# Kernel tuning notes

Measured on AMD Instinct MI355X. Metric: run time of the kernel, lower is better.

## Reference

```python
import jax, jax.numpy as jnp
import numpy as np

# ViT-B/16 CLIP visual tower dims
B, R, P = 32, 224, 16          # batch, resolution, patch
D, H, F, L = 768, 12, 3072, 12 # width, heads, mlp dim, layers
S = 1 + (R // P) ** 2          # 197 tokens (cls + patches)
O = 512                        # output proj dim
HD = D // H
MEAN = jnp.array([0.48145466, 0.4578275, 0.40821073], jnp.float32).reshape(1, 3, 1, 1)
STD = jnp.array([0.26862954, 0.26130258, 0.27577711], jnp.float32).reshape(1, 3, 1, 1)


def _ln(x, s, b):
    m = x.mean(-1, keepdims=True)
    v = ((x - m) ** 2).mean(-1, keepdims=True)
    return (x - m) * jax.lax.rsqrt(v + 1e-5) * s + b


def setup_inputs() -> dict:
    key = jax.random.key(0)
    ks = jax.random.split(key, 16)
    r = lambda i, shape: jax.random.normal(ks[i], shape, jnp.float32) * 0.02
    return dict(
        images=jax.random.uniform(ks[0], (B, 3, R, R), jnp.float32),
        conv_w=r(1, (D, 3, P, P)),
        cls_emb=r(2, (D,)),
        pos_emb=r(3, (S, D)),
        ln_pre_s=jnp.ones((D,), jnp.float32), ln_pre_b=jnp.zeros((D,), jnp.float32),
        ln1_s=jnp.ones((L, D), jnp.float32), ln1_b=jnp.zeros((L, D), jnp.float32),
        qkv_w=r(4, (L, 3 * D, D)), qkv_b=r(5, (L, 3 * D)),
        out_w=r(6, (L, D, D)), out_b=r(7, (L, D)),
        ln2_s=jnp.ones((L, D), jnp.float32), ln2_b=jnp.zeros((L, D), jnp.float32),
        fc_w=r(8, (L, F, D)), fc_b=r(9, (L, F)),
        proj_w=r(10, (L, D, F)), proj_b=r(11, (L, D)),
        ln_post_s=jnp.ones((D,), jnp.float32), ln_post_b=jnp.zeros((D,), jnp.float32),
        vis_proj=r(12, (D, O)),
    )


def reference(images, conv_w, cls_emb, pos_emb, ln_pre_s, ln_pre_b,
              ln1_s, ln1_b, qkv_w, qkv_b, out_w, out_b, ln2_s, ln2_b,
              fc_w, fc_b, proj_w, proj_b, ln_post_s, ln_post_b, vis_proj):
    x = (images - MEAN) / STD
    # conv1 patch embedding (no bias in CLIP): [B,D,14,14]
    x = jax.lax.conv_general_dilated(x, conv_w, (P, P), 'VALID',
                                     dimension_numbers=('NCHW', 'OIHW', 'NCHW'))
    x = x.reshape(B, D, -1).transpose(0, 2, 1)  # [B, 196, D]
    x = jnp.concatenate([jnp.broadcast_to(cls_emb, (B, 1, D)), x], axis=1) + pos_emb
    x = _ln(x, ln_pre_s, ln_pre_b)
    scale = HD ** -0.5

    def block(x, p):
        l1s, l1b, qw, qb, ow, ob, l2s, l2b, fw, fb, pw, pb = p
        h = _ln(x, l1s, l1b)
        qkv = h @ qw.T + qb                      # fused in_proj, [B,S,3D]
        q, k, v = jnp.split(qkv, 3, axis=-1)
        split = lambda t: t.reshape(B, S, H, HD).transpose(0, 2, 1, 3)
        q, k, v = split(q) * scale, split(k), split(v)
        attn = jax.nn.softmax(jnp.einsum('bhqd,bhkd->bhqk', q, k), axis=-1)
        o = jnp.einsum('bhqk,bhkd->bhqd', attn, v).transpose(0, 2, 1, 3).reshape(B, S, D)
        x = x + o @ ow.T + ob                    # out_proj + residual
        h = _ln(x, l2s, l2b) @ fw.T + fb
        h = h * jax.nn.sigmoid(1.702 * h)        # QuickGELU
        x = x + h @ pw.T + pb
        return x, None

    x, _ = jax.lax.scan(block, x, (ln1_s, ln1_b, qkv_w, qkv_b, out_w, out_b,
                                   ln2_s, ln2_b, fc_w, fc_b, proj_w, proj_b))
    x = _ln(x[:, 0], ln_post_s, ln_post_b)  # ln_post on cls token
    return x @ vis_proj                      # [B, 512]
```

## Files before the change

kernel.cpp:

```cpp
#include <hip/hip_runtime.h>
#include <cstddef>

#define Bv   32
#define Sv   197
#define Dv   768
#define Hh   12
#define HDv  64
#define Fv   3072
#define Lv   12
#define Ov   512
#define TOK  (Bv * Sv)
#define MPAD 6400
#define NPATCH 196
#define CONV_M (Bv * NPATCH)

#define WQ_SZ (2304 * 768)
#define WO_SZ (768 * 768)
#define WF_SZ (3072 * 768)
#define WP_SZ (768 * 3072)
#define WTOT  (WQ_SZ + WO_SZ + WF_SZ + WP_SZ)

typedef __attribute__((ext_vector_type(8))) __bf16 bf16x8;
typedef __attribute__((ext_vector_type(4))) float f32x4;

__device__ __forceinline__ unsigned short f2bf(float f) {
    unsigned int u = __float_as_uint(f);
    unsigned int r = (u + 0x7fffu + ((u >> 16) & 1u)) >> 16;
    return (unsigned short)r;
}

__device__ __forceinline__ void async_ld16(const void* g, void* l) {
    __builtin_amdgcn_global_load_lds(
        (__attribute__((address_space(1))) void*)(g),
        (__attribute__((address_space(3))) void*)(l),
        16, 0, 0);
}

__device__ __forceinline__ void reduce2_256(float& s1, float& s2) {
    #pragma unroll
    for (int off = 32; off > 0; off >>= 1) {
        s1 += __shfl_down(s1, off, 64);
        s2 += __shfl_down(s2, off, 64);
    }
    __shared__ float r1[4], r2[4];
    int lane = threadIdx.x & 63, w = threadIdx.x >> 6;
    if (lane == 0) { r1[w] = s1; r2[w] = s2; }
    __syncthreads();
    s1 = r1[0] + r1[1] + r1[2] + r1[3];
    s2 = r2[0] + r2[1] + r2[2] + r2[3];
    __syncthreads();
}

__global__ void convert_kernel(const float* __restrict__ src,
                               unsigned short* __restrict__ dst, int n4) {
    int gid = blockIdx.x * 256 + threadIdx.x;
    if (gid >= n4) return;
    int idx = gid * 4;
    float4 v = *(const float4*)(src + idx);
    ushort4 r = make_ushort4(f2bf(v.x), f2bf(v.y), f2bf(v.z), f2bf(v.w));
    *(ushort4*)(dst + idx) = r;
}

__global__ void convertw_kernel(const float* __restrict__ wq,
                                const float* __restrict__ wo,
                                const float* __restrict__ wf,
                                const float* __restrict__ wp,
                                unsigned short* __restrict__ dst) {
    int idx = (blockIdx.x * 256 + threadIdx.x) * 4;
    const float* s; int off;
    if (idx < WQ_SZ)                     { s = wq; off = idx; }
    else if (idx < WQ_SZ + WO_SZ)        { s = wo; off = idx - WQ_SZ; }
    else if (idx < WQ_SZ + WO_SZ + WF_SZ){ s = wf; off = idx - WQ_SZ - WO_SZ; }
    else                                 { s = wp; off = idx - WQ_SZ - WO_SZ - WF_SZ; }
    float4 v = *(const float4*)(s + off);
    ushort4 r = make_ushort4(f2bf(v.x), f2bf(v.y), f2bf(v.z), f2bf(v.w));
    *(ushort4*)(dst + idx) = r;
}

__global__ void im2col_kernel(const float* __restrict__ img,
                              unsigned short* __restrict__ out) {
    int idx = blockIdx.x * 256 + threadIdx.x;
    int col = idx % 768;
    int row = idx / 768;
    int b = row / NPATCH, p = row % NPATCH;
    int ph = p / 14, pw = p % 14;
    int c  = col >> 8;
    int r  = col & 255;
    int kh = r >> 4, kw = r & 15;
    int y = ph * 16 + kh, x = pw * 16 + kw;
    const float mean[3] = {0.48145466f, 0.4578275f, 0.40821073f};
    const float stdv[3] = {0.26862954f, 0.26130258f, 0.27577711f};
    float v = img[((size_t)(b * 3 + c) * 224 + y) * 224 + x];
    out[idx] = f2bf((v - mean[c]) / stdv[c]);
}

template<int ODT, int ACT>
__global__ __launch_bounds__(256) void gemm_mfma(
        const unsigned short* __restrict__ A, const unsigned short* __restrict__ W,
        const float* __restrict__ bias, const float* __restrict__ res,
        void* __restrict__ Cv, int M, int N, int K)
{
    __shared__ unsigned short As[128 * 32];
    __shared__ unsigned short Ws[128 * 32];
    const int tid = threadIdx.x;
    const int w = tid >> 6, l = tid & 63;
    const int m0 = blockIdx.y << 7, n0 = blockIdx.x << 7;

    const int srow = w * 32 + (l >> 2);
    const int scol = (l & 3) * 8;
    const unsigned short* ag0 = A + (size_t)(m0 + srow) * K + scol;
    const unsigned short* ag1 = ag0 + (size_t)16 * K;
    const unsigned short* wg0 = W + (size_t)(n0 + srow) * K + scol;
    const unsigned short* wg1 = wg0 + (size_t)16 * K;
    unsigned short* al0 = As + w * 1024;
    unsigned short* al1 = As + w * 1024 + 512;
    unsigned short* wl0 = Ws + w * 1024;
    unsigned short* wl1 = Ws + w * 1024 + 512;

    const int wm = w >> 1, wn = w & 1;
    const int fr = l & 15, fq = l >> 4;
    const unsigned short* afp[4];
    const unsigned short* wfp[4];
    #pragma unroll
    for (int i = 0; i < 4; i++) {
        afp[i] = As + (wm * 64 + i * 16 + fr) * 32 + fq * 8;
        wfp[i] = Ws + (wn * 64 + i * 16 + fr) * 32 + fq * 8;
    }

    f32x4 acc[4][4] = {};

    const int nk = K >> 5;
    for (int kk = 0; kk < nk; kk++) {
        const int ko = kk << 5;
        __syncthreads();
        async_ld16(ag0 + ko, al0);
        async_ld16(ag1 + ko, al1);
        async_ld16(wg0 + ko, wl0);
        async_ld16(wg1 + ko, wl1);
        __syncthreads();
        bf16x8 af[4], wf[4];
        #pragma unroll
        for (int i = 0; i < 4; i++) {
            af[i] = *(const bf16x8*)afp[i];
            wf[i] = *(const bf16x8*)wfp[i];
        }
        #pragma unroll
        for (int i = 0; i < 4; i++) {
            #pragma unroll
            for (int j = 0; j < 4; j++) {
                acc[i][j] = __builtin_amdgcn_mfma_f32_16x16x32_bf16(
                    af[i], wf[j], acc[i][j], 0, 0, 0);
            }
        }
    }

    float bn[4];
    #pragma unroll
    for (int j = 0; j < 4; j++)
        bn[j] = bias ? bias[n0 + wn * 64 + j * 16 + fr] : 0.f;

    #pragma unroll
    for (int i = 0; i < 4; i++) {
        #pragma unroll
        for (int r = 0; r < 4; r++) {
            int m = m0 + wm * 64 + i * 16 + fq * 4 + r;
            if (m < M) {
                size_t rowb = (size_t)m * N;
                #pragma unroll
                for (int j = 0; j < 4; j++) {
                    int n = n0 + wn * 64 + j * 16 + fr;
                    float v = acc[i][j][r] + bn[j];
                    if (res) v += res[rowb + n];
                    if (ACT) v = v / (1.f + __expf(-1.702f * v));
                    if (ODT == 0) ((float*)Cv)[rowb + n] = v;
                    else ((unsigned short*)Cv)[rowb + n] = f2bf(v);
                }
            }
        }
    }
}

__global__ void ln_kernel(const float* __restrict__ in, unsigned short* __restrict__ out,
                          const float* __restrict__ s, const float* __restrict__ b) {
    int t = blockIdx.x;
    const float* row = in + (size_t)t * Dv;
    int tid = threadIdx.x;
    float v[3], s1 = 0.f, s2 = 0.f;
    #pragma unroll
    for (int i = 0; i < 3; i++) {
        v[i] = row[tid + 256 * i];
        s1 += v[i]; s2 += v[i] * v[i];
    }
    reduce2_256(s1, s2);
    float mean = s1 * (1.0f / Dv);
    float var  = s2 * (1.0f / Dv) - mean * mean;
    float rstd = rsqrtf(var + 1e-5f);
    unsigned short* orow = out + (size_t)t * Dv;
    #pragma unroll
    for (int i = 0; i < 3; i++) {
        int d = tid + 256 * i;
        orow[d] = f2bf((v[i] - mean) * rstd * s[d] + b[d]);
    }
}

__global__ void embed_ln_kernel(const float* __restrict__ conv_out,
                                const float* __restrict__ cls,
                                const float* __restrict__ pos,
                                const float* __restrict__ s,
                                const float* __restrict__ b,
                                float* __restrict__ x) {
    int t = blockIdx.x;
    int bb = t / Sv, si = t % Sv;
    int tid = threadIdx.x;
    float v[3], s1 = 0.f, s2 = 0.f;
    #pragma unroll
    for (int i = 0; i < 3; i++) {
        int d = tid + 256 * i;
        float e = (si == 0) ? cls[d]
                            : conv_out[((size_t)bb * NPATCH + (si - 1)) * Dv + d];
        v[i] = e + pos[(size_t)si * Dv + d];
        s1 += v[i]; s2 += v[i] * v[i];
    }
    reduce2_256(s1, s2);
    float mean = s1 * (1.0f / Dv);
    float var  = s2 * (1.0f / Dv) - mean * mean;
    float rstd = rsqrtf(var + 1e-5f);
    float* orow = x + (size_t)t * Dv;
    #pragma unroll
    for (int i = 0; i < 3; i++) {
        int d = tid + 256 * i;
        orow[d] = (v[i] - mean) * rstd * s[d] + b[d];
    }
}

__global__ __launch_bounds__(256) void attn4_kernel(
        const unsigned short* __restrict__ qkv, unsigned short* __restrict__ o) {
    const int qg = blockIdx.x, h = blockIdx.y, b = blockIdx.z;
    __shared__ __align__(16) unsigned short vt[64][232];
    __shared__ __align__(16) unsigned short pb[32][236];
    __shared__ float red[4][32];
    __shared__ float smax_f[32];
    __shared__ float sinv_f[32];

    const int tid = threadIdx.x;
    const int w = tid >> 6, l = tid & 63;
    const int fr = l & 15, fq = l >> 4;
    const size_t base = (size_t)b * Sv;
    const unsigned int* q32 = (const unsigned int*)qkv;

    for (int i = tid; i < 224 * 32; i += 256) {
        int j = i >> 5, u = i & 31;
        unsigned int val = (j < Sv) ? q32[(base + j) * 1152 + 768 + h * 32 + u] : 0u;
        vt[2 * u][j]     = (unsigned short)(val & 0xffffu);
        vt[2 * u + 1][j] = (unsigned short)(val >> 16);
    }

    union U { uint4 u; bf16x8 v; };

    f32x4 sc[2][4] = {};
    #pragma unroll
    for (int ks = 0; ks < 2; ks++) {
        U aq[2];
        #pragma unroll
        for (int mt = 0; mt < 2; mt++) {
            int row = qg * 32 + mt * 16 + fr;
            int rc = row < Sv ? row : Sv - 1;
            aq[mt].u = *(const uint4*)(qkv + (base + rc) * 2304 + h * 64 + ks * 32 + fq * 8);
        }
        #pragma unroll
        for (int s = 0; s < 4; s++) {
            int nt = w + 4 * s;
            if (nt >= 14) continue;
            int col = nt * 16 + fr;
            int cc = col < Sv ? col : Sv - 1;
            U bq;
            bq.u = *(const uint4*)(qkv + (base + cc) * 2304 + 768 + h * 64 + ks * 32 + fq * 8);
            #pragma unroll
            for (int mt = 0; mt < 2; mt++)
                sc[mt][s] = __builtin_amdgcn_mfma_f32_16x16x32_bf16(
                    aq[mt].v, bq.v, sc[mt][s], 0, 0, 0);
        }
    }

    float rmax[2][4];
    #pragma unroll
    for (int mt = 0; mt < 2; mt++)
        #pragma unroll
        for (int r = 0; r < 4; r++) rmax[mt][r] = -1e30f;
    #pragma unroll
    for (int mt = 0; mt < 2; mt++) {
        #pragma unroll
        for (int s = 0; s < 4; s++) {
            int nt = w + 4 * s;
            int col = nt * 16 + fr;
            bool valid = (nt < 14) && (col < Sv);
            #pragma unroll
            for (int r = 0; r < 4; r++) {
                float v = valid ? sc[mt][s][r] * 0.125f : -1e30f;
                sc[mt][s][r] = v;
                rmax[mt][r] = fmaxf(rmax[mt][r], v);
            }
        }
    }
    #pragma unroll
    for (int mt = 0; mt < 2; mt++) {
        #pragma unroll
        for (int r = 0; r < 4; r++) {
            float m = rmax[mt][r];
            m = fmaxf(m, __shfl_xor(m, 1, 64));
            m = fmaxf(m, __shfl_xor(m, 2, 64));
            m = fmaxf(m, __shfl_xor(m, 4, 64));
            m = fmaxf(m, __shfl_xor(m, 8, 64));
            rmax[mt][r] = m;
        }
    }
    if (fr == 0) {
        #pragma unroll
        for (int mt = 0; mt < 2; mt++)
            #pragma unroll
            for (int r = 0; r < 4; r++)
                red[w][mt * 16 + fq * 4 + r] = rmax[mt][r];
    }
    __syncthreads();
    if (tid < 32)
        smax_f[tid] = fmaxf(fmaxf(red[0][tid], red[1][tid]),
                            fmaxf(red[2][tid], red[3][tid]));
    __syncthreads();

    float rsum[2][4] = {};
    #pragma unroll
    for (int mt = 0; mt < 2; mt++) {
        float fm[4];
        #pragma unroll
        for (int r = 0; r < 4; r++) fm[r] = smax_f[mt * 16 + fq * 4 + r];
        #pragma unroll
        for (int s = 0; s < 4; s++) {
            int nt = w + 4 * s;
            if (nt >= 14) continue;
            int col = nt * 16 + fr;
            #pragma unroll
            for (int r = 0; r < 4; r++) {
                float p = (col < Sv) ? __expf(sc[mt][s][r] - fm[r]) : 0.f;
                rsum[mt][r] += p;
                pb[mt * 16 + fq * 4 + r][col] = f2bf(p);
            }
        }
    }
    #pragma unroll
    for (int mt = 0; mt < 2; mt++) {
        #pragma unroll
        for (int r = 0; r < 4; r++) {
            float s = rsum[mt][r];
            s += __shfl_xor(s, 1, 64);
            s += __shfl_xor(s, 2, 64);
            s += __shfl_xor(s, 4, 64);
            s += __shfl_xor(s, 8, 64);
            rsum[mt][r] = s;
        }
    }
    if (fr == 0) {
        #pragma unroll
        for (int mt = 0; mt < 2; mt++)
            #pragma unroll
            for (int r = 0; r < 4; r++)
                red[w][mt * 16 + fq * 4 + r] = rsum[mt][r];
    }
    __syncthreads();
    if (tid < 32)
        sinv_f[tid] = 1.f / (red[0][tid] + red[1][tid] + red[2][tid] + red[3][tid]);
    __syncthreads();

    f32x4 oc[2] = {};
    #pragma unroll
    for (int ks = 0; ks < 7; ks++) {
        U bv;
        bv.u = *(const uint4*)&vt[w * 16 + fr][ks * 32 + fq * 8];
        #pragma unroll
        for (int mt = 0; mt < 2; mt++) {
            const unsigned short* ap = &pb[mt * 16 + fr][ks * 32 + fq * 8];
            uint2 lo = *(const uint2*)ap;
            uint2 hi = *(const uint2*)(ap + 4);
            U a; a.u = make_uint4(lo.x, lo.y, hi.x, hi.y);
            oc[mt] = __builtin_amdgcn_mfma_f32_16x16x32_bf16(a.v, bv.v, oc[mt], 0, 0, 0);
        }
    }

    #pragma unroll
    for (int mt = 0; mt < 2; mt++) {
        #pragma unroll
        for (int r = 0; r < 4; r++) {
            int lrow = mt * 16 + fq * 4 + r;
            int row = qg * 32 + lrow;
            if (row < Sv)
                o[(base + row) * Dv + h * 64 + w * 16 + fr] =
                    f2bf(oc[mt][r] * sinv_f[lrow]);
        }
    }
}

__global__ void head_kernel(const float* __restrict__ x,
                            const float* __restrict__ s, const float* __restrict__ b,
                            const float* __restrict__ vp, float* __restrict__ out) {
    int bb = blockIdx.x, tid = threadIdx.x;
    __shared__ float xn[Dv];
    const float* row = x + (size_t)(bb * Sv) * Dv;
    float v[3], s1 = 0.f, s2 = 0.f;
    #pragma unroll
    for (int i = 0; i < 3; i++) {
        v[i] = row[tid + 256 * i];
        s1 += v[i]; s2 += v[i] * v[i];
    }
    reduce2_256(s1, s2);
    float mean = s1 * (1.0f / Dv);
    float var  = s2 * (1.0f / Dv) - mean * mean;
    float rstd = rsqrtf(var + 1e-5f);
    #pragma unroll
    for (int i = 0; i < 3; i++) {
        int d = tid + 256 * i;
        xn[d] = (v[i] - mean) * rstd * s[d] + b[d];
    }
    __syncthreads();
    float acc0 = 0.f, acc1 = 0.f;
    for (int d = 0; d < Dv; d++) {
        float xv = xn[d];
        acc0 += xv * vp[(size_t)d * Ov + tid];
        acc1 += xv * vp[(size_t)d * Ov + tid + 256];
    }
    out[(size_t)bb * Ov + tid]       = acc0;
    out[(size_t)bb * Ov + tid + 256] = acc1;
}

extern "C" void kernel_launch(void* const* d_in, const int* in_sizes, int n_in,
                              void* d_out, int out_size, void* d_ws, size_t ws_size,
                              hipStream_t stream) {
    const float* images   = (const float*)d_in[0];
    const float* conv_w   = (const float*)d_in[1];
    const float* cls_emb  = (const float*)d_in[2];
    const float* pos_emb  = (const float*)d_in[3];
    const float* lnpre_s  = (const float*)d_in[4];
    const float* lnpre_b  = (const float*)d_in[5];
    const float* ln1_s    = (const float*)d_in[6];
    const float* ln1_b    = (const float*)d_in[7];
    const float* qkv_w    = (const float*)d_in[8];
    const float* qkv_b    = (const float*)d_in[9];
    const float* out_w    = (const float*)d_in[10];
    const float* out_b    = (const float*)d_in[11];
    const float* ln2_s    = (const float*)d_in[12];
    const float* ln2_b    = (const float*)d_in[13];
    const float* fc_w     = (const float*)d_in[14];
    const float* fc_b     = (const float*)d_in[15];
    const float* proj_w   = (const float*)d_in[16];
    const float* proj_b   = (const float*)d_in[17];
    const float* lnpost_s = (const float*)d_in[18];
    const float* lnpost_b = (const float*)d_in[19];
    const float* vis_proj = (const float*)d_in[20];
    float* out = (float*)d_out;

    char* p = (char*)d_ws;
    float* x              = (float*)p;          p += (size_t)TOK * Dv * 4;
    unsigned short* abuf  = (unsigned short*)p; p += (size_t)MPAD * Dv * 2;
    unsigned short* qkvb  = (unsigned short*)p; p += (size_t)MPAD * 2304 * 2;
    unsigned short* hbuf  = (unsigned short*)p; p += (size_t)MPAD * Fv * 2;
    unsigned short* wbuf  = (unsigned short*)p; p += (size_t)WTOT * 2;
    unsigned short* cwb   = (unsigned short*)p; p += (size_t)WO_SZ * 2;
    unsigned short* im2c  = qkvb;
    float* convo          = (float*)hbuf;

    convert_kernel<<<WO_SZ / 4 / 256, 256, 0, stream>>>(conv_w, cwb, WO_SZ / 4);
    im2col_kernel<<<(CONV_M * Dv) / 256, 256, 0, stream>>>(images, im2c);
    gemm_mfma<0, 0><<<dim3(Dv / 128, CONV_M / 128), 256, 0, stream>>>(
        im2c, cwb, nullptr, nullptr, convo, CONV_M, Dv, Dv);
    embed_ln_kernel<<<TOK, 256, 0, stream>>>(convo, cls_emb, pos_emb,
                                             lnpre_s, lnpre_b, x);

    unsigned short* wq = wbuf;
    unsigned short* wo = wbuf + WQ_SZ;
    unsigned short* wf = wbuf + WQ_SZ + WO_SZ;
    unsigned short* wp = wbuf + WQ_SZ + WO_SZ + WF_SZ;
    const int GM = MPAD / 128;

    for (int l = 0; l < Lv; l++) {
        convertw_kernel<<<WTOT / 4 / 256, 256, 0, stream>>>(
            qkv_w + (size_t)l * WQ_SZ, out_w + (size_t)l * WO_SZ,
            fc_w + (size_t)l * WF_SZ, proj_w + (size_t)l * WP_SZ, wbuf);
        ln_kernel<<<TOK, 256, 0, stream>>>(x, abuf, ln1_s + l * Dv, ln1_b + l * Dv);
        gemm_mfma<1, 0><<<dim3(2304 / 128, GM), 256, 0, stream>>>(
            abuf, wq, qkv_b + (size_t)l * 2304, nullptr, qkvb, TOK, 2304, Dv);
        attn4_kernel<<<dim3(7, Hh, Bv), 256, 0, stream>>>(qkvb, abuf);
        gemm_mfma<0, 0><<<dim3(Dv / 128, GM), 256, 0, stream>>>(
            abuf, wo, out_b + (size_t)l * Dv, x, x, TOK, Dv, Dv);
        ln_kernel<<<TOK, 256, 0, stream>>>(x, abuf, ln2_s + l * Dv, ln2_b + l * Dv);
        gemm_mfma<1, 1><<<dim3(Fv / 128, GM), 256, 0, stream>>>(
            abuf, wf, fc_b + (size_t)l * Fv, nullptr, hbuf, TOK, Fv, Dv);
        gemm_mfma<0, 0><<<dim3(Dv / 128, GM), 256, 0, stream>>>(
            hbuf, wp, proj_b + (size_t)l * Dv, x, x, TOK, Dv, Fv);
    }

    head_kernel<<<Bv, 256, 0, stream>>>(x, lnpost_s, lnpost_b, vis_proj, out);
}
```

Measured before the change: 4.344 ms.

## Double-buffer GEMM LDS tiles and swizzle workgroups across XCDs

```diff
diff --git a/kernel.cpp b/kernel.cpp
--- a/kernel.cpp
+++ b/kernel.cpp
@@ -100,11 +100,19 @@
         const float* __restrict__ bias, const float* __restrict__ res,
         void* __restrict__ Cv, int M, int N, int K)
 {
-    __shared__ unsigned short As[128 * 32];
-    __shared__ unsigned short Ws[128 * 32];
+    __shared__ unsigned short As[2][128 * 32];
+    __shared__ unsigned short Ws[2][128 * 32];
     const int tid = threadIdx.x;
     const int w = tid >> 6, l = tid & 63;
-    const int m0 = blockIdx.y << 7, n0 = blockIdx.x << 7;
+
+    const int gx = gridDim.x;
+    const int wg  = blockIdx.y * gx + blockIdx.x;
+    const int nwg = gx * gridDim.y;
+    const int q = nwg >> 3, r8 = nwg & 7;
+    const int xcd = wg & 7, lo = wg >> 3;
+    const int swz = (xcd < r8 ? xcd * (q + 1) : r8 * (q + 1) + (xcd - r8) * q) + lo;
+    const int m0 = (swz / gx) << 7;
+    const int n0 = (swz % gx) << 7;
 
     const int srow = w * 32 + (l >> 2);
     const int scol = (l & 3) * 8;
@@ -112,37 +120,42 @@
     const unsigned short* ag1 = ag0 + (size_t)16 * K;
     const unsigned short* wg0 = W + (size_t)(n0 + srow) * K + scol;
     const unsigned short* wg1 = wg0 + (size_t)16 * K;
-    unsigned short* al0 = As + w * 1024;
-    unsigned short* al1 = As + w * 1024 + 512;
-    unsigned short* wl0 = Ws + w * 1024;
-    unsigned short* wl1 = Ws + w * 1024 + 512;
 
     const int wm = w >> 1, wn = w & 1;
     const int fr = l & 15, fq = l >> 4;
-    const unsigned short* afp[4];
-    const unsigned short* wfp[4];
+    int aoff[4], woff[4];
     #pragma unroll
     for (int i = 0; i < 4; i++) {
-        afp[i] = As + (wm * 64 + i * 16 + fr) * 32 + fq * 8;
-        wfp[i] = Ws + (wn * 64 + i * 16 + fr) * 32 + fq * 8;
+        aoff[i] = (wm * 64 + i * 16 + fr) * 32 + fq * 8;
+        woff[i] = (wn * 64 + i * 16 + fr) * 32 + fq * 8;
     }
 
     f32x4 acc[4][4] = {};
-
     const int nk = K >> 5;
+
+    async_ld16(ag0, &As[0][w * 1024]);
+    async_ld16(ag1, &As[0][w * 1024 + 512]);
+    async_ld16(wg0, &Ws[0][w * 1024]);
+    async_ld16(wg1, &Ws[0][w * 1024 + 512]);
+
+    int cur = 0;
     for (int kk = 0; kk < nk; kk++) {
-        const int ko = kk << 5;
         __syncthreads();
-        async_ld16(ag0 + ko, al0);
-        async_ld16(ag1 + ko, al1);
-        async_ld16(wg0 + ko, wl0);
-        async_ld16(wg1 + ko, wl1);
-        __syncthreads();
+        if (kk + 1 < nk) {
+            const int ko = (kk + 1) << 5;
+            const int nb = cur ^ 1;
+            async_ld16(ag0 + ko, &As[nb][w * 1024]);
+            async_ld16(ag1 + ko, &As[nb][w * 1024 + 512]);
+            async_ld16(wg0 + ko, &Ws[nb][w * 1024]);
+            async_ld16(wg1 + ko, &Ws[nb][w * 1024 + 512]);
+        }
+        const unsigned short* ab = As[cur];
+        const unsigned short* wb = Ws[cur];
         bf16x8 af[4], wf[4];
         #pragma unroll
         for (int i = 0; i < 4; i++) {
-            af[i] = *(const bf16x8*)afp[i];
-            wf[i] = *(const bf16x8*)wfp[i];
+            af[i] = *(const bf16x8*)(ab + aoff[i]);
+            wf[i] = *(const bf16x8*)(wb + woff[i]);
         }
         #pragma unroll
         for (int i = 0; i < 4; i++) {
@@ -152,6 +165,7 @@
                     af[i], wf[j], acc[i][j], 0, 0, 0);
             }
         }
+        cur ^= 1;
     }
 
     float bn[4];
```

After: 4.114 ms. -5.3%, faster.
